# Optimization experiments

Hardware: AMD Instinct MI355X
Metric: run time of the kernel (lower is better)

## Reference

```python
import jax, jax.numpy as jnp
import numpy as np

TEMPERATURE = 8.0  # sqrt(head_dim=64)


def setup_inputs() -> dict:
    key = jax.random.key(0)
    kq, kk, kv, km = jax.random.split(key, 4)
    B, S, D = 16, 2048, 64
    q = jax.random.normal(kq, (B, S, D), dtype=jnp.float32)
    k = jax.random.normal(kk, (B, S, D), dtype=jnp.float32)
    v = jax.random.normal(kv, (B, S, D), dtype=jnp.float32)
    mask = jax.random.randint(km, (B, S, S), 0, 2).astype(jnp.bool_)
    return {"q": q, "k": k, "v": v, "mask": mask}


def reference(q, k, v, mask):
    # latent = q @ k^T / temperature  -> [B, Sq, Sk]
    latent = jnp.einsum('bqd,bkd->bqk', q, k) / TEMPERATURE
    # NOTE: the original fills masked positions with 1e-9 (NOT -inf); keep faithful.
    latent = jnp.where(mask, jnp.float32(1e-9), latent)
    attn = jax.nn.softmax(latent, axis=-1)
    return jnp.einsum('bqk,bkd->bqd', attn, v)
```

## Files before the change

kernel.cpp:

```cpp
#include <hip/hip_runtime.h>
#include <hip/hip_bf16.h>

#define BB 16
#define SS 2048
#define DD 64
#define NT (SS / 64)

typedef __attribute__((ext_vector_type(8)))  unsigned short ushort8;
typedef __attribute__((ext_vector_type(8)))  __bf16 bf16x8;
typedef __attribute__((ext_vector_type(16))) float f32x16;

static __device__ __forceinline__ unsigned short f2bf(float x) {
    return __builtin_bit_cast(unsigned short, __float2bfloat16(x));
}
static __device__ __forceinline__ unsigned pk2f(float a, float b) {
    return (unsigned)f2bf(a) | ((unsigned)f2bf(b) << 16);
}
union F4 { float4 v; float a[4]; };

__global__ __launch_bounds__(256, 2)
void sdpa_mfma_kernel(const float* __restrict__ Q, const float* __restrict__ K,
                      const float* __restrict__ V, const unsigned int* __restrict__ M,
                      float* __restrict__ O) {
    __shared__ __align__(16) char smem[8192 + 4 * 5120];
    char* Qs = smem;

    const int t    = threadIdx.x;
    const int lane = t & 63;
    const int l31  = lane & 31;
    const int half = lane >> 5;
    const int w    = t >> 6;
    const int qs   = w & 1;
    const int kh   = w >> 1;
    const int b    = blockIdx.y;
    const int q0   = blockIdx.x * 64;
    char* Vw = smem + 8192 + w * 5120;

    const float* Qg = Q + ((size_t)b * SS + q0) * DD;
    const float* Kg = K + (size_t)b * SS * DD;
    const float* Vg = V + (size_t)b * SS * DD;
    const unsigned int* Mg = M + (size_t)b * SS * SS + (size_t)q0 * SS;

    const int gk  = lane >> 4;
    const int d0v = (lane & 15) * 4;
    const float* kp = Kg + (size_t)(32 * kh + l31) * DD + 8 * half;
    const float* vp = Vg + (size_t)(32 * kh + 8 * gk) * DD + d0v;
    const unsigned int* mp = Mg + (size_t)(32 * qs + l31) * SS + 32 * kh + 4 * half;

    F4 kf[8], vf[8];
    uint4 mfA[4], mfB[4];

    #pragma unroll
    for (int dc = 0; dc < 4; dc++) {
        kf[2 * dc].v     = *(const float4*)(kp + 16 * dc);
        kf[2 * dc + 1].v = *(const float4*)(kp + 16 * dc + 4);
    }
    #pragma unroll
    for (int r = 0; r < 8; r++) vf[r].v = *(const float4*)(vp + r * DD);
    #pragma unroll
    for (int g = 0; g < 4; g++) mfA[g] = *(const uint4*)(mp + 8 * g);

    {
        const int sr = t >> 2, scm = t & 3;
        F4 f0, f1, f2, f3;
        const float* src = Qg + sr * DD + scm * 16;
        f0.v = *(const float4*)(src);
        f1.v = *(const float4*)(src + 4);
        f2.v = *(const float4*)(src + 8);
        f3.v = *(const float4*)(src + 12);
        ushort8 u0, u1;
        #pragma unroll
        for (int e = 0; e < 4; e++) {
            u0[e]     = f2bf(f0.a[e] * 0.125f);
            u0[e + 4] = f2bf(f1.a[e] * 0.125f);
            u1[e]     = f2bf(f2.a[e] * 0.125f);
            u1[e + 4] = f2bf(f3.a[e] * 0.125f);
        }
        *(ushort8*)(Qs + sr * 128 + (((scm * 2)     ^ (sr & 7)) * 16)) = u0;
        *(ushort8*)(Qs + sr * 128 + (((scm * 2 + 1) ^ (sr & 7)) * 16)) = u1;
    }
    __syncthreads();

    const int qrow = 32 * qs + l31;
    bf16x8 bq[4];
    #pragma unroll
    for (int dc = 0; dc < 4; dc++)
        bq[dc] = __builtin_bit_cast(bf16x8, *(const ushort8*)(
            Qs + qrow * 128 + (((2 * dc + half) ^ (qrow & 7)) * 16)));

    f32x16 On0, On1;
    #pragma unroll
    for (int i = 0; i < 16; i++) { On0[i] = 0.f; On1[i] = 0.f; }
    float den_acc = 0.f;

#define ITER(MC, MN, KT) do {                                                  \
    const int ktn_ = ((KT) + 1 < NT) ? (KT) + 1 : NT - 1;                      \
            \
    {                                                                          \
        const unsigned int* mpp_ = mp + (size_t)ktn_ * 64;                     \
        _Pragma("unroll")                                                      \
        for (int g = 0; g < 4; g++) MN[g] = *(const uint4*)(mpp_ + 8 * g);     \
    }                                                                          \
                                   \
    bf16x8 ak_[4];                                                             \
    _Pragma("unroll")                                                          \
    for (int dc = 0; dc < 4; dc++) {                                           \
        ushort8 u_;                                                            \
        _Pragma("unroll")                                                      \
        for (int e = 0; e < 4; e++) {                                          \
            u_[e]     = f2bf(kf[2 * dc].a[e]);                                 \
            u_[e + 4] = f2bf(kf[2 * dc + 1].a[e]);                             \
        }                                                                      \
        ak_[dc] = __builtin_bit_cast(bf16x8, u_);                              \
    }                                                                          \
                                            \
    f32x16 S_;                                                                 \
    _Pragma("unroll")                                                          \
    for (int i = 0; i < 16; i++) S_[i] = 0.f;                                  \
    _Pragma("unroll")                                                          \
    for (int dc = 0; dc < 4; dc++)                                             \
        S_ = __builtin_amdgcn_mfma_f32_32x32x16_bf16(ak_[dc], bq[dc], S_, 0, 0, 0); \
                             \
    float p_[16];                                                              \
    _Pragma("unroll")                                                          \
    for (int g = 0; g < 4; g++) {                                              \
        const unsigned mw_[4] = {MC[g].x, MC[g].y, MC[g].z, MC[g].w};          \
        _Pragma("unroll")                                                      \
        for (int e = 0; e < 4; e++) {                                          \
            const float ev_ = __expf(S_[4 * g + e]);                           \
            const float pv_ = mw_[e] ? 1.0f : ev_;                             \
            p_[4 * g + e] = pv_;                                               \
            den_acc += pv_;                                                    \
        }                                                                      \
    }                                                                          \
        \
    _Pragma("unroll")                                                          \
    for (int e = 0; e < 4; e++) {                                              \
        const int d_ = d0v + e;                                                \
        uint4 pkv_;                                                            \
        pkv_.x = pk2f(vf[0].a[e], vf[1].a[e]);                                 \
        pkv_.y = pk2f(vf[2].a[e], vf[3].a[e]);                                 \
        pkv_.z = pk2f(vf[4].a[e], vf[5].a[e]);                                 \
        pkv_.w = pk2f(vf[6].a[e], vf[7].a[e]);                                 \
        *(uint4*)(Vw + d_ * 80 + (((gk ^ (d_ >> 2)) & 3) * 16)) = pkv_;        \
    }                                                                          \
                               \
    {                                                                          \
        const float* kpp_ = kp + (size_t)ktn_ * 4096;                          \
        _Pragma("unroll")                                                      \
        for (int dc = 0; dc < 4; dc++) {                                       \
            kf[2 * dc].v     = *(const float4*)(kpp_ + 16 * dc);               \
            kf[2 * dc + 1].v = *(const float4*)(kpp_ + 16 * dc + 4);           \
        }                                                                      \
        const float* vpp_ = vp + (size_t)ktn_ * 4096;                          \
        _Pragma("unroll")                                                      \
        for (int r = 0; r < 8; r++) vf[r].v = *(const float4*)(vpp_ + r * DD); \
    }                                                                          \
                          \
    _Pragma("unroll")                                                          \
    for (int s2 = 0; s2 < 2; s2++) {                                           \
        const unsigned o0 = pk2f(p_[8 * s2 + 0], p_[8 * s2 + 1]);              \
        const unsigned o1 = pk2f(p_[8 * s2 + 2], p_[8 * s2 + 3]);              \
        const unsigned o2 = pk2f(p_[8 * s2 + 4], p_[8 * s2 + 5]);              \
        const unsigned o3 = pk2f(p_[8 * s2 + 6], p_[8 * s2 + 7]);              \
        const unsigned s0 = half ? o0 : o2;                                    \
        const unsigned s1 = half ? o1 : o3;                                    \
        const unsigned r0 = (unsigned)__shfl_xor((int)s0, 32, 64);             \
        const unsigned r1 = (unsigned)__shfl_xor((int)s1, 32, 64);             \
        uint4 bu;                                                              \
        bu.x = half ? r0 : o0;                                                 \
        bu.y = half ? r1 : o1;                                                 \
        bu.z = half ? o2 : r0;                                                 \
        bu.w = half ? o3 : r1;                                                 \
        const bf16x8 bp = __builtin_bit_cast(bf16x8, bu);                      \
        _Pragma("unroll")                                                      \
        for (int dc2 = 0; dc2 < 2; dc2++) {                                    \
            const int vrow = 32 * dc2 + l31;                                   \
            bf16x8 av = __builtin_bit_cast(bf16x8, *(const ushort8*)(          \
                Vw + vrow * 80 + ((((2 * s2 + half) ^ (vrow >> 2)) & 3) * 16))); \
            if (dc2 == 0) On0 = __builtin_amdgcn_mfma_f32_32x32x16_bf16(av, bp, On0, 0, 0, 0); \
            else          On1 = __builtin_amdgcn_mfma_f32_32x32x16_bf16(av, bp, On1, 0, 0, 0); \
        }                                                                      \
    }                                                                          \
} while (0)

    for (int kt = 0; kt < NT; kt += 2) {
        ITER(mfA, mfB, kt);
        ITER(mfB, mfA, kt + 1);
    }
#undef ITER

    const float den_tot = den_acc + __shfl_xor(den_acc, 32, 64);
    float* red  = (float*)smem;
    float* denx = (float*)(smem + 16384);

    __syncthreads();
    if (kh == 1) {
        #pragma unroll
        for (int dc = 0; dc < 2; dc++)
            #pragma unroll
            for (int g = 0; g < 4; g++) {
                const f32x16& Oc = dc ? On1 : On0;
                float4 st;
                st.x = Oc[4 * g + 0]; st.y = Oc[4 * g + 1];
                st.z = Oc[4 * g + 2]; st.w = Oc[4 * g + 3];
                *(float4*)((char*)red + qs * 8192 + (dc * 4 + g) * 1024 + lane * 16) = st;
            }
        if (lane < 32) denx[qs * 32 + l31] = den_tot;
    }
    __syncthreads();
    if (kh == 0) {
        const float inv = 1.0f / (den_tot + denx[qs * 32 + l31]);
        float* Og = O + ((size_t)b * SS + q0 + qrow) * DD;
        #pragma unroll
        for (int dc = 0; dc < 2; dc++)
            #pragma unroll
            for (int g = 0; g < 4; g++) {
                const float4 pr = *(const float4*)((char*)red + qs * 8192 + (dc * 4 + g) * 1024 + lane * 16);
                const f32x16& Oc = dc ? On1 : On0;
                float4 st;
                st.x = (Oc[4 * g + 0] + pr.x) * inv;
                st.y = (Oc[4 * g + 1] + pr.y) * inv;
                st.z = (Oc[4 * g + 2] + pr.z) * inv;
                st.w = (Oc[4 * g + 3] + pr.w) * inv;
                *(float4*)(Og + 32 * dc + 8 * g + 4 * half) = st;
            }
    }
}

extern "C" void kernel_launch(void* const* d_in, const int* in_sizes, int n_in,
                              void* d_out, int out_size, void* d_ws, size_t ws_size,
                              hipStream_t stream) {
    const float* q = (const float*)d_in[0];
    const float* k = (const float*)d_in[1];
    const float* v = (const float*)d_in[2];
    const unsigned int* m = (const unsigned int*)d_in[3];
    float* out = (float*)d_out;

    dim3 grid(SS / 64, BB);
    sdpa_mfma_kernel<<<grid, 256, 0, stream>>>(q, k, v, m, out);
}
```

Before: 437.4 us.

## Split keys across four waves with 32-query blocks and earlier K prefetch

Each block now handles 32 queries instead of 64. Its four waves each take a contiguous quarter of the key range instead of splitting queries two ways and interleaving key halves. The grid doubles, launch bounds request 4 blocks per CU, and the K prefetch moves ahead of the QK MFMA. At the end, three partial outputs and denominators are reduced through LDS. The aim is more parallelism and better latency hiding on the mask and K/V loads, at the cost of reading K/V twice as often per query and a larger final cross-wave reduction.

```diff
diff --git a/kernel.cpp b/kernel.cpp
--- a/kernel.cpp
+++ b/kernel.cpp
@@ -4,7 +4,7 @@
 #define BB 16
 #define SS 2048
 #define DD 64
-#define NT (SS / 64)
+#define NIT 16
 
 typedef __attribute__((ext_vector_type(8)))  unsigned short ushort8;
 typedef __attribute__((ext_vector_type(8)))  __bf16 bf16x8;
@@ -18,34 +18,30 @@
 }
 union F4 { float4 v; float a[4]; };
 
-__global__ __launch_bounds__(256, 2)
+__global__ __launch_bounds__(256, 4)
 void sdpa_mfma_kernel(const float* __restrict__ Q, const float* __restrict__ K,
                       const float* __restrict__ V, const unsigned int* __restrict__ M,
                       float* __restrict__ O) {
-    __shared__ __align__(16) char smem[8192 + 4 * 5120];
+    __shared__ __align__(16) char smem[25088];
     char* Qs = smem;
 
     const int t    = threadIdx.x;
     const int lane = t & 63;
     const int l31  = lane & 31;
     const int half = lane >> 5;
-    const int w    = t >> 6;
-    const int qs   = w & 1;
-    const int kh   = w >> 1;
+    const int kh   = t >> 6;
     const int b    = blockIdx.y;
-    const int q0   = blockIdx.x * 64;
-    char* Vw = smem + 8192 + w * 5120;
+    const int q0   = blockIdx.x * 32;
+    char* Vw = smem + 4096 + kh * 5120;
 
     const float* Qg = Q + ((size_t)b * SS + q0) * DD;
-    const float* Kg = K + (size_t)b * SS * DD;
-    const float* Vg = V + (size_t)b * SS * DD;
     const unsigned int* Mg = M + (size_t)b * SS * SS + (size_t)q0 * SS;
 
     const int gk  = lane >> 4;
     const int d0v = (lane & 15) * 4;
-    const float* kp = Kg + (size_t)(32 * kh + l31) * DD + 8 * half;
-    const float* vp = Vg + (size_t)(32 * kh + 8 * gk) * DD + d0v;
-    const unsigned int* mp = Mg + (size_t)(32 * qs + l31) * SS + 32 * kh + 4 * half;
+    const float* kp = K + ((size_t)b * SS + 512 * kh + l31) * DD + 8 * half;
+    const float* vp = V + ((size_t)b * SS + 512 * kh + 8 * gk) * DD + d0v;
+    const unsigned int* mp = Mg + (size_t)l31 * SS + 512 * kh + 4 * half;
 
     F4 kf[8], vf[8];
     uint4 mfA[4], mfB[4];
@@ -61,27 +57,20 @@
     for (int g = 0; g < 4; g++) mfA[g] = *(const uint4*)(mp + 8 * g);
 
     {
-        const int sr = t >> 2, scm = t & 3;
-        F4 f0, f1, f2, f3;
-        const float* src = Qg + sr * DD + scm * 16;
-        f0.v = *(const float4*)(src);
-        f1.v = *(const float4*)(src + 4);
-        f2.v = *(const float4*)(src + 8);
-        f3.v = *(const float4*)(src + 12);
-        ushort8 u0, u1;
+        const int sr = t >> 3, sc = t & 7;
+        const float* src = Qg + sr * DD + sc * 8;
+        F4 f0, f1; f0.v = *(const float4*)src; f1.v = *(const float4*)(src + 4);
+        ushort8 u;
         #pragma unroll
         for (int e = 0; e < 4; e++) {
-            u0[e]     = f2bf(f0.a[e] * 0.125f);
-            u0[e + 4] = f2bf(f1.a[e] * 0.125f);
-            u1[e]     = f2bf(f2.a[e] * 0.125f);
-            u1[e + 4] = f2bf(f3.a[e] * 0.125f);
+            u[e]     = f2bf(f0.a[e] * 0.125f);
+            u[e + 4] = f2bf(f1.a[e] * 0.125f);
         }
-        *(ushort8*)(Qs + sr * 128 + (((scm * 2)     ^ (sr & 7)) * 16)) = u0;
-        *(ushort8*)(Qs + sr * 128 + (((scm * 2 + 1) ^ (sr & 7)) * 16)) = u1;
+        *(ushort8*)(Qs + sr * 128 + ((sc ^ (sr & 7)) * 16)) = u;
     }
     __syncthreads();
 
-    const int qrow = 32 * qs + l31;
+    const int qrow = l31;
     bf16x8 bq[4];
     #pragma unroll
     for (int dc = 0; dc < 4; dc++)
@@ -94,10 +83,10 @@
     float den_acc = 0.f;
 
 #define ITER(MC, MN, KT) do {                                                  \
-    const int ktn_ = ((KT) + 1 < NT) ? (KT) + 1 : NT - 1;                      \
-            \
+    const int ktn_ = ((KT) + 1 < NIT) ? (KT) + 1 : NIT - 1;                    \
+                      \
     {                                                                          \
-        const unsigned int* mpp_ = mp + (size_t)ktn_ * 64;                     \
+        const unsigned int* mpp_ = mp + ktn_ * 32;                             \
         _Pragma("unroll")                                                      \
         for (int g = 0; g < 4; g++) MN[g] = *(const uint4*)(mpp_ + 8 * g);     \
     }                                                                          \
@@ -112,6 +101,15 @@
             u_[e + 4] = f2bf(kf[2 * dc + 1].a[e]);                             \
         }                                                                      \
         ak_[dc] = __builtin_bit_cast(bf16x8, u_);                              \
+    }                                                                          \
+             \
+    {                                                                          \
+        const float* kpp_ = kp + (size_t)ktn_ * 2048;                          \
+        _Pragma("unroll")                                                      \
+        for (int dc = 0; dc < 4; dc++) {                                       \
+            kf[2 * dc].v     = *(const float4*)(kpp_ + 16 * dc);               \
+            kf[2 * dc + 1].v = *(const float4*)(kpp_ + 16 * dc + 4);           \
+        }                                                                      \
     }                                                                          \
                                             \
     f32x16 S_;                                                                 \
@@ -144,15 +142,9 @@
         pkv_.w = pk2f(vf[6].a[e], vf[7].a[e]);                                 \
         *(uint4*)(Vw + d_ * 80 + (((gk ^ (d_ >> 2)) & 3) * 16)) = pkv_;        \
     }                                                                          \
-                               \
+                                           \
     {                                                                          \
-        const float* kpp_ = kp + (size_t)ktn_ * 4096;                          \
-        _Pragma("unroll")                                                      \
-        for (int dc = 0; dc < 4; dc++) {                                       \
-            kf[2 * dc].v     = *(const float4*)(kpp_ + 16 * dc);               \
-            kf[2 * dc + 1].v = *(const float4*)(kpp_ + 16 * dc + 4);           \
-        }                                                                      \
-        const float* vpp_ = vp + (size_t)ktn_ * 4096;                          \
+        const float* vpp_ = vp + (size_t)ktn_ * 2048;                          \
         _Pragma("unroll")                                                      \
         for (int r = 0; r < 8; r++) vf[r].v = *(const float4*)(vpp_ + r * DD); \
     }                                                                          \
@@ -184,7 +176,7 @@
     }                                                                          \
 } while (0)
 
-    for (int kt = 0; kt < NT; kt += 2) {
+    for (int kt = 0; kt < NIT; kt += 2) {
         ITER(mfA, mfB, kt);
         ITER(mfB, mfA, kt + 1);
     }
@@ -192,10 +184,10 @@
 
     const float den_tot = den_acc + __shfl_xor(den_acc, 32, 64);
     float* red  = (float*)smem;
-    float* denx = (float*)(smem + 16384);
+    float* denx = (float*)(smem + 24576);
 
     __syncthreads();
-    if (kh == 1) {
+    if (kh != 0) {
         #pragma unroll
         for (int dc = 0; dc < 2; dc++)
             #pragma unroll
@@ -204,25 +196,29 @@
                 float4 st;
                 st.x = Oc[4 * g + 0]; st.y = Oc[4 * g + 1];
                 st.z = Oc[4 * g + 2]; st.w = Oc[4 * g + 3];
-                *(float4*)((char*)red + qs * 8192 + (dc * 4 + g) * 1024 + lane * 16) = st;
+                *(float4*)((char*)red + (kh - 1) * 8192 + (dc * 4 + g) * 1024 + lane * 16) = st;
             }
-        if (lane < 32) denx[qs * 32 + l31] = den_tot;
+        if (lane < 32) denx[kh * 32 + l31] = den_tot;
     }
     __syncthreads();
     if (kh == 0) {
-        const float inv = 1.0f / (den_tot + denx[qs * 32 + l31]);
+        const float inv = 1.0f / (den_tot + denx[32 + l31] + denx[64 + l31] + denx[96 + l31]);
         float* Og = O + ((size_t)b * SS + q0 + qrow) * DD;
         #pragma unroll
         for (int dc = 0; dc < 2; dc++)
             #pragma unroll
             for (int g = 0; g < 4; g++) {
-                const float4 pr = *(const float4*)((char*)red + qs * 8192 + (dc * 4 + g) * 1024 + lane * 16);
                 const f32x16& Oc = dc ? On1 : On0;
                 float4 st;
-                st.x = (Oc[4 * g + 0] + pr.x) * inv;
-                st.y = (Oc[4 * g + 1] + pr.y) * inv;
-                st.z = (Oc[4 * g + 2] + pr.z) * inv;
-                st.w = (Oc[4 * g + 3] + pr.w) * inv;
+                st.x = Oc[4 * g + 0]; st.y = Oc[4 * g + 1];
+                st.z = Oc[4 * g + 2]; st.w = Oc[4 * g + 3];
+                #pragma unroll
+                for (int w2 = 0; w2 < 3; w2++) {
+                    const float4 pr = *(const float4*)((char*)red + w2 * 8192 +
+                                                       (dc * 4 + g) * 1024 + lane * 16);
+                    st.x += pr.x; st.y += pr.y; st.z += pr.z; st.w += pr.w;
+                }
+                st.x *= inv; st.y *= inv; st.z *= inv; st.w *= inv;
                 *(float4*)(Og + 32 * dc + 8 * g + 4 * half) = st;
             }
     }
@@ -237,6 +233,6 @@
     const unsigned int* m = (const unsigned int*)d_in[3];
     float* out = (float*)d_out;
 
-    dim3 grid(SS / 64, BB);
+    dim3 grid(SS / 32, BB);
     sdpa_mfma_kernel<<<grid, 256, 0, stream>>>(q, k, v, m, out);
 }
```

Result: slower. 598.8 us (+36.9%).
